# Kernel tuning notes

Hardware: AMD Instinct MI355X
Metric: run time of the kernel (lower is better)

The kernel has to match this reference:

```python
import jax, jax.numpy as jnp
import numpy as np

N_NODES = 100000


def gcn_conv(x, edge_index, W, b):
    """PyG-style GCNConv: h = D^-1/2 (A+I) D^-1/2 (x W) + b."""
    n = x.shape[0]
    loop = jnp.arange(n)
    src = jnp.concatenate([edge_index[0], loop])  # [E+N]
    dst = jnp.concatenate([edge_index[1], loop])  # [E+N]
    # degree computed on destination nodes (PyG gcn_norm with self-loops)
    deg = jnp.zeros((n,), x.dtype).at[dst].add(1.0)
    dinv = jnp.where(deg > 0, jax.lax.rsqrt(deg), 0.0)
    norm = dinv[src] * dinv[dst]  # [E+N]
    h = x @ W  # [n, out]
    msg = h[src] * norm[:, None]  # gather + scale
    out = jax.ops.segment_sum(msg, dst, num_segments=n)  # scatter-add
    return out + b


def setup_inputs() -> dict:
    key = jax.random.key(0)
    ks = jax.random.split(key, 8)
    F_in, H, C = 64, 64, 32
    x = jax.random.normal(ks[0], (N_NODES, F_in), dtype=jnp.float32)
    edge_index = jax.random.randint(ks[1], (2, 1200000), 0, N_NODES, dtype=jnp.int64)
    W1 = jax.random.normal(ks[2], (F_in, H), dtype=jnp.float32) / np.sqrt(F_in)
    b1 = jnp.zeros((H,), jnp.float32)
    W2 = jax.random.normal(ks[3], (H, H), dtype=jnp.float32) / np.sqrt(H)
    b2 = jnp.zeros((H,), jnp.float32)
    Wc = jax.random.normal(ks[4], (H, C), dtype=jnp.float32) / np.sqrt(H)
    bc = jnp.zeros((C,), jnp.float32)
    return {"x": x, "edge_index": edge_index, "W1": W1, "b1": b1,
            "W2": W2, "b2": b2, "Wc": Wc, "bc": bc}


def reference(x, edge_index, W1, b1, W2, b2, Wc, bc):
    h = jnp.tanh(gcn_conv(x, edge_index, W1, b1))
    h = jnp.tanh(gcn_conv(h, edge_index, W2, b2))
    out = h @ Wc + bc
    return (out, h)
```

## Files before the change

kernel.cpp:

```cpp
#include <hip/hip_runtime.h>
#include <hip/hip_bf16.h>
#include <stdint.h>

#define CB_SHIFT 11
#define CB_NODES 2048
#define CAP 28672
#define PT 4096

static __device__ inline uint16_t f2bf(float f) {
    union { float f; uint32_t u; } v; v.f = f;
    uint32_t r = v.u + 0x7FFFu + ((v.u >> 16) & 1u);
    return (uint16_t)(r >> 16);
}
static __device__ inline float bflo(uint32_t u) {
    union { uint32_t u; float f; } v; v.u = u << 16; return v.f;
}
static __device__ inline float bfhi(uint32_t u) {
    union { uint32_t u; float f; } v; v.u = u & 0xFFFF0000u; return v.f;
}
static __device__ inline float tanh_fast(float x) {
    x = fminf(fmaxf(x, -20.f), 20.f);
    float e = __expf(2.f * x);
    return fmaf(-2.f, __builtin_amdgcn_rcpf(e + 1.f), 1.f);
}

__global__ __launch_bounds__(256) void k_init(const uint32_t* __restrict__ e, int E,
                                              int* __restrict__ flag, int* __restrict__ gcur,
                                              int* __restrict__ dhist) {
    int t = threadIdx.x;
    dhist[t] = 0;
    if (t < 64) {
        gcur[t] = 0;
        int cnt = E < 1024 ? E : 1024;
        int nz = 0;
        for (int i = t; i < cnt; i += 64) nz |= (e[2 * i + 1] != 0u);
        int any = __any(nz);
        if (t == 0) *flag = any ? 0 : 1;
    }
}

__global__ __launch_bounds__(256) void k_part(const uint32_t* __restrict__ e, int E,
                                              const int* __restrict__ flag,
                                              int* __restrict__ gcur,
                                              uint32_t* __restrict__ parts) {
    __shared__ int sh_hist[64], sh_off[64], sh_base[64];
    __shared__ uint32_t sh_buf[PT];
    __shared__ uint16_t sh_bkt[PT];
    int t = threadIdx.x;
    int tile0 = blockIdx.x * PT;
    int is64 = *flag;
    if (t < 64) sh_hist[t] = 0;
    __syncthreads();

    uint32_t rec[16]; int cb[16], rank[16];
    const uint2* e2p = (const uint2*)e;
    for (int j = 0; j < 16; ++j) {
        int idx = tile0 + j * 256 + t;
        cb[j] = -1;
        if (idx < E) {
            uint32_t s, d;
            if (is64) { s = e2p[idx].x; d = e2p[E + idx].x; }
            else      { s = e[idx];     d = e[E + idx]; }
            rec[j] = (s << CB_SHIFT) | (d & (CB_NODES - 1));
            cb[j] = (int)(d >> CB_SHIFT);
            rank[j] = atomicAdd(&sh_hist[cb[j]], 1);
        }
    }
    __syncthreads();
    if (t < 64) {
        int cnt = sh_hist[t];
        int incl = cnt;
        for (int o = 1; o < 64; o <<= 1) {
            int v = __shfl_up(incl, o);
            if (t >= o) incl += v;
        }
        sh_off[t] = incl - cnt;
        sh_base[t] = (cnt > 0) ? atomicAdd(&gcur[t], cnt) : 0;
    }
    __syncthreads();
    for (int j = 0; j < 16; ++j) {
        if (cb[j] >= 0) {
            int slot = sh_off[cb[j]] + rank[j];
            sh_buf[slot] = rec[j];
            sh_bkt[slot] = (uint16_t)cb[j];
        }
    }
    __syncthreads();
    int total = min(PT, E - tile0);
    for (int i = t; i < total; i += 256) {
        int b = sh_bkt[i];
        int dest = sh_base[b] + (i - sh_off[b]);
        parts[(size_t)b * CAP + dest] = sh_buf[i];
    }
}

__global__ __launch_bounds__(1024) void k_build(const uint32_t* __restrict__ parts,
                                                const int* __restrict__ gcur,
                                                float* __restrict__ dinv,
                                                int* __restrict__ rowbeg,
                                                int* __restrict__ rowend,
                                                uint32_t* __restrict__ col,
                                                int* __restrict__ dhist, int N) {
    __shared__ int hist[CB_NODES], cur[CB_NODES], wsum[16], dh[256];
    int t = threadIdx.x, cb = blockIdx.x;
    int lane = t & 63, w = t >> 6;
    for (int i = t; i < CB_NODES; i += 1024) hist[i] = 0;
    if (t < 256) dh[t] = 0;
    __syncthreads();
    int cnt = gcur[cb];
    const uint32_t* rp = parts + (size_t)cb * CAP;
    for (int i = t; i < cnt; i += 1024) atomicAdd(&hist[rp[i] & (CB_NODES - 1)], 1);
    __syncthreads();
    int h0 = hist[2 * t], h1 = hist[2 * t + 1];
    int n0 = cb * CB_NODES;
    if (n0 + 2 * t < N)     atomicAdd(&dh[min(h0, 255)], 1);
    if (n0 + 2 * t + 1 < N) atomicAdd(&dh[min(h1, 255)], 1);
    int s = h0 + h1;
    int incl = s;
    for (int o = 1; o < 64; o <<= 1) {
        int v = __shfl_up(incl, o);
        if (lane >= o) incl += v;
    }
    if (lane == 63) wsum[w] = incl;
    __syncthreads();
    if (t < 16) {
        int v = wsum[t];
        int inc2 = v;
        for (int o = 1; o < 16; o <<= 1) {
            int u = __shfl_up(inc2, o);
            if (t >= o) inc2 += u;
        }
        wsum[t] = inc2 - v;
    }
    __syncthreads();
    int ex = wsum[w] + incl - s;
    int b0 = ex, b1 = ex + h0;
    cur[2 * t] = b0;
    cur[2 * t + 1] = b1;
    int base = cb * CAP;
    if (n0 + 2 * t < N) {
        rowbeg[n0 + 2 * t] = base + b0;
        rowend[n0 + 2 * t] = base + b0 + h0;
        dinv[n0 + 2 * t] = rsqrtf((float)(h0 + 1));
    }
    if (n0 + 2 * t + 1 < N) {
        rowbeg[n0 + 2 * t + 1] = base + b1;
        rowend[n0 + 2 * t + 1] = base + b1 + h1;
        dinv[n0 + 2 * t + 1] = rsqrtf((float)(h1 + 1));
    }
    __syncthreads();
    if (t < 256 && dh[t]) atomicAdd(&dhist[t], dh[t]);
    for (int i = t; i < cnt; i += 1024) {
        uint32_t rec = rp[i];
        int pos = atomicAdd(&cur[rec & (CB_NODES - 1)], 1);
        col[base + pos] = rec >> CB_SHIFT;
    }
}

__global__ __launch_bounds__(256) void k_dscan(const int* __restrict__ dhist,
                                               int* __restrict__ dcur) {
    __shared__ int sd[256];
    int t = threadIdx.x;
    int v = dhist[t];
    sd[t] = v; __syncthreads();
    for (int o = 1; o < 256; o <<= 1) {
        int x = (t >= o) ? sd[t - o] : 0;
        __syncthreads();
        sd[t] += x;
        __syncthreads();
    }
    dcur[t] = sd[t] - v;
}

__global__ __launch_bounds__(1024) void k_dperm(const int* __restrict__ rowbeg,
                                                const int* __restrict__ rowend,
                                                const float* __restrict__ dinv,
                                                int* __restrict__ dcur,
                                                int4* __restrict__ perm4, int N) {
    __shared__ int lh[256], lbase[256];
    int t = threadIdx.x;
    if (t < 256) lh[t] = 0;
    __syncthreads();
    int n = blockIdx.x * 1024 + t;
    int c = 0, rank = 0, beg = 0, deg = 0;
    if (n < N) {
        beg = rowbeg[n];
        deg = rowend[n] - beg;
        c = min(deg, 255);
        rank = atomicAdd(&lh[c], 1);
    }
    __syncthreads();
    if (t < 256 && lh[t]) lbase[t] = atomicAdd(&dcur[t], lh[t]);
    __syncthreads();
    if (n < N) {
        int pos = lbase[c] + rank;
        perm4[pos] = make_int4(beg, deg, n, __float_as_int(dinv[n]));
    }
}

__global__ __launch_bounds__(256) void k_gemm(const float* __restrict__ A,
                                              const float* __restrict__ W,
                                              const float* __restrict__ dinv,
                                              uint16_t* __restrict__ out, int N) {
    __shared__ __align__(16) float xT[64 * 68];
    __shared__ __align__(16) float Wl[64 * 64];
    int t = threadIdx.x;
#pragma unroll
    for (int j = 0; j < 16; ++j) Wl[j * 256 + t] = W[j * 256 + t];
    int n0 = blockIdx.x * 64;
    int nvalid = min(64, N - n0);
#pragma unroll
    for (int j = 0; j < 4; ++j) {
        int flat = j * 256 + t;
        int node = flat >> 4;
        int k4 = (flat & 15) * 4;
        float4 v = make_float4(0.f, 0.f, 0.f, 0.f);
        if (node < nvalid) v = *(const float4*)&A[(size_t)(n0 + node) * 64 + k4];
        xT[(k4 + 0) * 68 + node] = v.x;
        xT[(k4 + 1) * 68 + node] = v.y;
        xT[(k4 + 2) * 68 + node] = v.z;
        xT[(k4 + 3) * 68 + node] = v.w;
    }
    __syncthreads();
    int ng = t >> 4, cg = t & 15;
    float acc[4][4] = {};
#pragma unroll 8
    for (int k = 0; k < 64; ++k) {
        float4 a = *(const float4*)&xT[k * 68 + 4 * ng];
        float4 b = *(const float4*)&Wl[k * 64 + 4 * cg];
        float av[4] = {a.x, a.y, a.z, a.w};
        float bv[4] = {b.x, b.y, b.z, b.w};
#pragma unroll
        for (int i = 0; i < 4; ++i)
#pragma unroll
            for (int j = 0; j < 4; ++j) acc[i][j] = fmaf(av[i], bv[j], acc[i][j]);
    }
#pragma unroll
    for (int i = 0; i < 4; ++i) {
        int ln = 4 * ng + i;
        if (ln < nvalid) {
            int n = n0 + ln;
            float dv = dinv[n];
            ushort4 o;
            o.x = f2bf(acc[i][0] * dv);
            o.y = f2bf(acc[i][1] * dv);
            o.z = f2bf(acc[i][2] * dv);
            o.w = f2bf(acc[i][3] * dv);
            *(ushort4*)&out[(size_t)n * 64 + 4 * cg] = o;
        }
    }
}

__global__ __launch_bounds__(512) void k_agg(const uint16_t* __restrict__ h,
                                             const int4* __restrict__ perm4,
                                             const uint32_t* __restrict__ col,
                                             const float* __restrict__ bias,
                                             float* __restrict__ out, int N) {
    int t = threadIdx.x;
    int lane = t & 63, wid = t >> 6;
    int slot = lane >> 3;
    int g = lane & 7;
    const uint4* hp = (const uint4*)h;
    float bv[8];
#pragma unroll
    for (int j = 0; j < 8; ++j) bv[j] = bias[g * 8 + j];
    int idx = (blockIdx.x * 8 + wid) * 8 + slot;
    bool valid = idx < N;
    int4 pi = make_int4(0, 0, 0, 0);
    if (valid) pi = perm4[idx];
    int rs = pi.x, deg = valid ? pi.y : 0, n = pi.z;
    float di = __int_as_float(pi.w);
    int m = deg;
#pragma unroll
    for (int o = 1; o < 64; o <<= 1) m = max(m, __shfl_xor(m, o));
    float acc[8] = {};
#pragma unroll 4
    for (int it = 0; it < m; ++it) {
        if (it < deg) {
            int src = (int)col[rs + it];
            uint4 v = hp[(size_t)src * 8 + g];
            acc[0] += bflo(v.x); acc[1] += bfhi(v.x);
            acc[2] += bflo(v.y); acc[3] += bfhi(v.y);
            acc[4] += bflo(v.z); acc[5] += bfhi(v.z);
            acc[6] += bflo(v.w); acc[7] += bfhi(v.w);
        }
    }
    if (valid) {
        uint4 v = hp[(size_t)n * 8 + g];
        float hn[8] = {bflo(v.x), bfhi(v.x), bflo(v.y), bfhi(v.y),
                       bflo(v.z), bfhi(v.z), bflo(v.w), bfhi(v.w)};
        __align__(16) float o[8];
#pragma unroll
        for (int j = 0; j < 8; ++j)
            o[j] = tanh_fast(di * (acc[j] + hn[j]) + bv[j]);
        *(float4*)&out[(size_t)n * 64 + g * 8]     = *(float4*)&o[0];
        *(float4*)&out[(size_t)n * 64 + g * 8 + 4] = *(float4*)&o[4];
    }
}

__global__ __launch_bounds__(256) void k_cls(const float* __restrict__ A,
                                             const float* __restrict__ W,
                                             const float* __restrict__ bc,
                                             float* __restrict__ out, int N) {
    __shared__ __align__(16) float xT[64 * 68];
    __shared__ __align__(16) float Wl[64 * 32];
    int t = threadIdx.x;
#pragma unroll
    for (int j = 0; j < 8; ++j) Wl[j * 256 + t] = W[j * 256 + t];
    int n0 = blockIdx.x * 64;
    int nvalid = min(64, N - n0);
#pragma unroll
    for (int j = 0; j < 4; ++j) {
        int flat = j * 256 + t;
        int node = flat >> 4;
        int k4 = (flat & 15) * 4;
        float4 v = make_float4(0.f, 0.f, 0.f, 0.f);
        if (node < nvalid) v = *(const float4*)&A[(size_t)(n0 + node) * 64 + k4];
        xT[(k4 + 0) * 68 + node] = v.x;
        xT[(k4 + 1) * 68 + node] = v.y;
        xT[(k4 + 2) * 68 + node] = v.z;
        xT[(k4 + 3) * 68 + node] = v.w;
    }
    __syncthreads();
    int ng = t >> 4, cg = t & 15;
    float acc[4][2] = {};
#pragma unroll 8
    for (int k = 0; k < 64; ++k) {
        float4 a = *(const float4*)&xT[k * 68 + 4 * ng];
        float2 b = *(const float2*)&Wl[k * 32 + 2 * cg];
        float av[4] = {a.x, a.y, a.z, a.w};
#pragma unroll
        for (int i = 0; i < 4; ++i) {
            acc[i][0] = fmaf(av[i], b.x, acc[i][0]);
            acc[i][1] = fmaf(av[i], b.y, acc[i][1]);
        }
    }
    float2 bcv = *(const float2*)&bc[2 * cg];
#pragma unroll
    for (int i = 0; i < 4; ++i) {
        int ln = 4 * ng + i;
        if (ln < nvalid) {
            int n = n0 + ln;
            float2 o = make_float2(acc[i][0] + bcv.x, acc[i][1] + bcv.y);
            *(float2*)&out[(size_t)n * 32 + 2 * cg] = o;
        }
    }
}

extern "C" void kernel_launch(void* const* d_in, const int* in_sizes, int n_in,
                              void* d_out, int out_size, void* d_ws, size_t ws_size,
                              hipStream_t stream) {
    const float*    x     = (const float*)d_in[0];
    const uint32_t* edges = (const uint32_t*)d_in[1];
    const float*    W1    = (const float*)d_in[2];
    const float*    b1    = (const float*)d_in[3];
    const float*    W2    = (const float*)d_in[4];
    const float*    b2    = (const float*)d_in[5];
    const float*    Wc    = (const float*)d_in[6];
    const float*    bc    = (const float*)d_in[7];

    const int N   = in_sizes[0] / 64;
    const int E   = in_sizes[1] / 2;
    const int NBC = (N + CB_NODES - 1) >> CB_SHIFT;
    const int NTG = (N + 63) / 64;
    const int NTP = (E + PT - 1) / PT;
    const int NAG = (N + 63) / 64;
    const int NDP = (N + 1023) / 1024;

    char* w = (char*)d_ws;
    size_t off = 0;
    auto alloc = [&](size_t bytes) {
        void* p = w + off;
        off = (off + bytes + 255) & ~(size_t)255;
        return p;
    };
    int*      flag   = (int*)alloc(4);
    int*      gcur   = (int*)alloc(64 * 4);
    int*      dhist  = (int*)alloc(256 * 4);
    int*      dcur   = (int*)alloc(256 * 4);
    float*    dinv   = (float*)alloc((size_t)N * 4);
    uint32_t* parts  = (uint32_t*)alloc((size_t)NBC * CAP * 4);
    uint32_t* col    = (uint32_t*)alloc((size_t)NBC * CAP * 4);
    int*      rowbeg = (int*)alloc((size_t)N * 4);
    int*      rowend = (int*)alloc((size_t)N * 4);
    int4*     perm4  = (int4*)alloc((size_t)N * 16);
    uint16_t* bufA   = (uint16_t*)alloc((size_t)N * 64 * 2);

    float* outc = (float*)d_out;
    float* hfin = outc + (size_t)N * 32;

    hipLaunchKernelGGL(k_init, dim3(1), dim3(256), 0, stream, edges, E, flag, gcur, dhist);
    hipLaunchKernelGGL(k_part, dim3(NTP), dim3(256), 0, stream, edges, E, flag, gcur, parts);
    hipLaunchKernelGGL(k_build, dim3(NBC), dim3(1024), 0, stream, parts, gcur, dinv, rowbeg, rowend, col, dhist, N);
    hipLaunchKernelGGL(k_dscan, dim3(1), dim3(256), 0, stream, dhist, dcur);
    hipLaunchKernelGGL(k_dperm, dim3(NDP), dim3(1024), 0, stream, rowbeg, rowend, dinv, dcur, perm4, N);

    hipLaunchKernelGGL(k_gemm, dim3(NTG), dim3(256), 0, stream, x, W1, dinv, bufA, N);
    hipLaunchKernelGGL(k_agg, dim3(NAG), dim3(512), 0, stream, bufA, perm4, col, b1, hfin, N);
    hipLaunchKernelGGL(k_gemm, dim3(NTG), dim3(256), 0, stream, hfin, W2, dinv, bufA, N);
    hipLaunchKernelGGL(k_agg, dim3(NAG), dim3(512), 0, stream, bufA, perm4, col, b2, hfin, N);
    hipLaunchKernelGGL(k_cls, dim3(NTG), dim3(256), 0, stream, hfin, Wc, bc, outc, N);
}
```

Measured before the change: 260.6 us.

## Split each node's edge list across two lane groups and reverse degree order

The aggregation kernel now gives each destination node 16 lanes instead of 8. The two 8-lane halves walk alternate edges, and their partial sums are combined with a cross-lane shuffle. Each half then finishes and writes 4 of the 8 output features. The degree-sorted permutation is written in reverse, so high-degree nodes are scheduled first and the long-tail work runs early. The aim is to halve the serial loop length per node and cut load imbalance, at the cost of twice as many blocks and an extra shuffle reduction.

Measured after the change: 255.5 us. About the same (-1.9%).

```diff
diff --git a/kernel.cpp b/kernel.cpp
--- a/kernel.cpp
+++ b/kernel.cpp
@@ -194,7 +194,7 @@
     __syncthreads();
     if (n < N) {
         int pos = lbase[c] + rank;
-        perm4[pos] = make_int4(beg, deg, n, __float_as_int(dinv[n]));
+        perm4[(N - 1) - pos] = make_int4(beg, deg, n, __float_as_int(dinv[n]));
     }
 }
 
@@ -258,13 +258,14 @@
                                              float* __restrict__ out, int N) {
     int t = threadIdx.x;
     int lane = t & 63, wid = t >> 6;
-    int slot = lane >> 3;
+    int slot = lane >> 4;
+    int sub  = (lane >> 3) & 1;
     int g = lane & 7;
     const uint4* hp = (const uint4*)h;
-    float bv[8];
-#pragma unroll
-    for (int j = 0; j < 8; ++j) bv[j] = bias[g * 8 + j];
-    int idx = (blockIdx.x * 8 + wid) * 8 + slot;
+    float bv[4];
+#pragma unroll
+    for (int j = 0; j < 4; ++j) bv[j] = bias[g * 8 + sub * 4 + j];
+    int idx = (blockIdx.x * 8 + wid) * 4 + slot;
     bool valid = idx < N;
     int4 pi = make_int4(0, 0, 0, 0);
     if (valid) pi = perm4[idx];
@@ -273,11 +274,13 @@
     int m = deg;
 #pragma unroll
     for (int o = 1; o < 64; o <<= 1) m = max(m, __shfl_xor(m, o));
+    int trips = (m + 1) >> 1;
     float acc[8] = {};
 #pragma unroll 4
-    for (int it = 0; it < m; ++it) {
-        if (it < deg) {
-            int src = (int)col[rs + it];
+    for (int it = 0; it < trips; ++it) {
+        int e = 2 * it + sub;
+        if (e < deg) {
+            int src = (int)col[rs + e];
             uint4 v = hp[(size_t)src * 8 + g];
             acc[0] += bflo(v.x); acc[1] += bfhi(v.x);
             acc[2] += bflo(v.y); acc[3] += bfhi(v.y);
@@ -285,16 +288,21 @@
             acc[6] += bflo(v.w); acc[7] += bfhi(v.w);
         }
     }
+#pragma unroll
+    for (int j = 0; j < 8; ++j) acc[j] += __shfl_xor(acc[j], 8);
     if (valid) {
-        uint4 v = hp[(size_t)n * 8 + g];
-        float hn[8] = {bflo(v.x), bfhi(v.x), bflo(v.y), bfhi(v.y),
-                       bflo(v.z), bfhi(v.z), bflo(v.w), bfhi(v.w)};
-        __align__(16) float o[8];
-#pragma unroll
-        for (int j = 0; j < 8; ++j)
-            o[j] = tanh_fast(di * (acc[j] + hn[j]) + bv[j]);
-        *(float4*)&out[(size_t)n * 64 + g * 8]     = *(float4*)&o[0];
-        *(float4*)&out[(size_t)n * 64 + g * 8 + 4] = *(float4*)&o[4];
+        float s0 = sub ? acc[4] : acc[0];
+        float s1 = sub ? acc[5] : acc[1];
+        float s2 = sub ? acc[6] : acc[2];
+        float s3 = sub ? acc[7] : acc[3];
+        uint2 v = *(const uint2*)&h[(size_t)n * 64 + g * 8 + sub * 4];
+        float hn0 = bflo(v.x), hn1 = bfhi(v.x), hn2 = bflo(v.y), hn3 = bfhi(v.y);
+        __align__(16) float o[4];
+        o[0] = tanh_fast(di * (s0 + hn0) + bv[0]);
+        o[1] = tanh_fast(di * (s1 + hn1) + bv[1]);
+        o[2] = tanh_fast(di * (s2 + hn2) + bv[2]);
+        o[3] = tanh_fast(di * (s3 + hn3) + bv[3]);
+        *(float4*)&out[(size_t)n * 64 + g * 8 + sub * 4] = *(float4*)&o[0];
     }
 }
 
@@ -364,7 +372,7 @@
     const int NBC = (N + CB_NODES - 1) >> CB_SHIFT;
     const int NTG = (N + 63) / 64;
     const int NTP = (E + PT - 1) / PT;
-    const int NAG = (N + 63) / 64;
+    const int NAG = (N + 31) / 32;
     const int NDP = (N + 1023) / 1024;
 
     char* w = (char*)d_ws;
```
